# Kernel optimization log

Measured on AMD Instinct MI355X. Metric: run time of the kernel, lower is better.

Reference implementation:

```python
import jax, jax.numpy as jnp
import numpy as np

NUM_HEADS = 12
DIM_HEAD = 32
EMBED_DIM = NUM_HEADS * DIM_HEAD  # 384
EPS = 1e-5


def _channel_layernorm(x, w, b):
    # LayerNorm over channel axis (axis=1) of [B, D, S, L], per spatial position
    mu = jnp.mean(x, axis=1, keepdims=True)
    var = jnp.mean(jnp.square(x - mu), axis=1, keepdims=True)
    xn = (x - mu) / jnp.sqrt(var + EPS)
    return xn * w[None, :, None, None] + b[None, :, None, None]


def _qkv(x, w, b):
    # 1x1 conv == per-position matmul: [3D, D] x [B, D, S, L] -> [B, 3D, S, L]
    B, D, S, L = x.shape
    y = jnp.einsum('od,bdsl->bosl', w, x) + b[None, :, None, None]
    q, k, v = jnp.split(y, 3, axis=1)
    shp = (B, NUM_HEADS, DIM_HEAD, S, L)
    return q.reshape(shp), k.reshape(shp), v.reshape(shp)


def setup_inputs() -> dict:
    key = jax.random.key(0)
    ks = jax.random.split(key, 5)
    B, D, S, L = 1, EMBED_DIM, 128, 256
    x = jax.random.normal(ks[0], (B, D, S, L), dtype=jnp.float32)
    row_w = jax.random.normal(ks[1], (3 * D, D), dtype=jnp.float32) * (D ** -0.5)
    row_b = jax.random.normal(ks[2], (3 * D,), dtype=jnp.float32) * 0.02
    col_w = jax.random.normal(ks[3], (3 * D, D), dtype=jnp.float32) * (D ** -0.5)
    col_b = jax.random.normal(ks[4], (3 * D,), dtype=jnp.float32) * 0.02
    return {
        'x': x,
        'row_w': row_w, 'row_b': row_b,
        'col_w': col_w, 'col_b': col_b,
        'ln1_w': jnp.ones((D,), jnp.float32), 'ln1_b': jnp.zeros((D,), jnp.float32),
        'ln2_w': jnp.ones((D,), jnp.float32), 'ln2_b': jnp.zeros((D,), jnp.float32),
    }


def reference(x, row_w, row_b, col_w, col_b, ln1_w, ln1_b, ln2_w, ln2_b):
    B, D, S, L = x.shape
    # --- row attention (attend across L within each row s) ---
    q, k, v = _qkv(x, row_w, row_b)  # [B,H,C,S,L]
    row_attn = jnp.einsum('bhcsi,bhcsj->bhsij', q, k)  # note: no 1/sqrt(d) scaling (faithful)
    row_attn = jax.nn.softmax(row_attn, axis=-1)
    row_out = jnp.einsum('bhsij,bhdsj->bhdsi', row_attn, v).reshape(B, D, S, L)
    out = _channel_layernorm(x + row_out, ln1_w, ln1_b)
    # --- column attention (attend across S within each column l) ---
    q, k, v = _qkv(out, col_w, col_b)
    col_attn = jnp.einsum('bhcil,bhcjl->bhijl', q, k)
    col_attn = jax.nn.softmax(col_attn, axis=-2)
    col_out = jnp.einsum('bhijl,bhdjl->bhdil', col_attn, v).reshape(B, D, S, L)
    out = _channel_layernorm(out + col_out, ln2_w, ln2_b)
    return out
```

## Files before the change

kernel.cpp:

```cpp
#include <hip/hip_runtime.h>
#include <math.h>

#define DCH 384
#define NH 12
#define CH 32
#define SS 128
#define LL 256
#define NPOS 32768
#define THREE_D 1152

typedef _Float16 f16_t;
typedef _Float16 f16x4 __attribute__((ext_vector_type(4)));
typedef _Float16 f16x8 __attribute__((ext_vector_type(8)));
typedef float f32x4 __attribute__((ext_vector_type(4)));

#define GLD16(gptr, lptr) __builtin_amdgcn_global_load_lds( \
    (const __attribute__((address_space(1))) unsigned int*)(gptr), \
    (__attribute__((address_space(3))) unsigned int*)(lptr), 16, 0, 0)

#define WAVE_LDS_FENCE() __asm__ volatile("s_waitcnt lgkmcnt(0)" ::: "memory")

__global__ __launch_bounds__(256) void conv_w(const float* __restrict__ in,
                                              f16_t* __restrict__ out, int n4) {
    int i = blockIdx.x * 256 + threadIdx.x;
    if (i < n4) {
        float4 v = ((const float4*)in)[i];
        unsigned short u0 = __builtin_bit_cast(unsigned short, (f16_t)v.x);
        unsigned short u1 = __builtin_bit_cast(unsigned short, (f16_t)v.y);
        unsigned short u2 = __builtin_bit_cast(unsigned short, (f16_t)v.z);
        unsigned short u3 = __builtin_bit_cast(unsigned short, (f16_t)v.w);
        uint2 r;
        r.x = (unsigned)u0 | ((unsigned)u1 << 16);
        r.y = (unsigned)u2 | ((unsigned)u3 << 16);
        ((uint2*)out)[i] = r;
    }
}

__global__ __launch_bounds__(256) void zero_stats(float* __restrict__ p) {
    ((float4*)p)[blockIdx.x * 256 + threadIdx.x] = (float4){0.f, 0.f, 0.f, 0.f};
}

__global__ __launch_bounds__(256) void conv_xT(const float* __restrict__ in,
                                               f16_t* __restrict__ outp) {
    __shared__ float tile[64][65];
    const int p0 = blockIdx.x * 64;
    const int k0 = blockIdx.y * 64;
    const int tx = threadIdx.x & 63, ty = threadIdx.x >> 6;
#pragma unroll
    for (int i = 0; i < 16; ++i)
        tile[ty * 16 + i][tx] = in[(size_t)(k0 + ty * 16 + i) * NPOS + p0 + tx];
    __syncthreads();
    const int pr = threadIdx.x >> 2;
    const int cg = threadIdx.x & 3;
    union { uint4 v[2]; unsigned int u[8]; } res;
#pragma unroll
    for (int j = 0; j < 8; ++j) {
        unsigned short lo = __builtin_bit_cast(unsigned short, (f16_t)tile[cg * 16 + 2 * j][pr]);
        unsigned short hi = __builtin_bit_cast(unsigned short, (f16_t)tile[cg * 16 + 2 * j + 1][pr]);
        res.u[j] = (unsigned)lo | ((unsigned)hi << 16);
    }
    uint4* dst = (uint4*)&outp[(size_t)(p0 + pr) * DCH + k0 + cg * 16];
    dst[0] = res.v[0];
    dst[1] = res.v[1];
}

__global__ __launch_bounds__(512) void qkv_gemm_f16(
        const f16_t* __restrict__ Wh,
        const float* __restrict__ bias,
        const f16_t* __restrict__ Xp,
        f16_t* __restrict__ Yq, f16_t* __restrict__ Yk, f16_t* __restrict__ Yv)
{
    __shared__ f16_t sha[128 * 384];
    const int tid  = threadIdx.x;
    const int lane = tid & 63;
    const int wave = tid >> 6;

    const int hwid = blockIdx.y * 9 + blockIdx.x;
    const int nid  = (hwid & 7) * 144 + (hwid >> 3);
    const int ot   = nid % 9;
    const int pt   = nid / 9;
    const int o0 = ot * 128;
    const int p0 = pt * 256;

    const int mrow = lane & 15;
    const int kgq  = lane >> 4;

#pragma unroll
    for (int j = 0; j < 12; ++j) {
        const int ibase = (wave * 12 + j) * 64;
        const int i = ibase + lane;
        const int row = i / 48;
        const int s = i - row * 48;
        const int g = s ^ (row & 7);
        GLD16(Wh + (size_t)(o0 + row) * DCH + g * 8, sha + (size_t)ibase * 8);
    }

    const f16_t* bp0 = Xp + (size_t)(p0 + wave * 32 + mrow) * DCH + kgq * 8;
    const f16_t* bp1 = bp0 + (size_t)16 * DCH;

    f32x4 acc[8][2] = {};
    f16x8 breg[3][2];

    breg[0][0] = *(const f16x8*)(bp0);
    breg[0][1] = *(const f16x8*)(bp1);
    breg[1][0] = *(const f16x8*)(bp0 + 32);
    breg[1][1] = *(const f16x8*)(bp1 + 32);

    __syncthreads();

    const int key = mrow & 7;
    constexpr int NK = DCH / 32;
#pragma unroll
    for (int t = 0; t < NK; ++t) {
        if (t + 2 < NK) {
            breg[(t + 2) % 3][0] = *(const f16x8*)(bp0 + (t + 2) * 32);
            breg[(t + 2) % 3][1] = *(const f16x8*)(bp1 + (t + 2) * 32);
        }
        const int soff = ((t * 4 + kgq) ^ key) * 8;
#pragma unroll
        for (int mi = 0; mi < 8; ++mi) {
            const f16x8 a = *(const f16x8*)(sha + (size_t)(mi * 16 + mrow) * DCH + soff);
            acc[mi][0] = __builtin_amdgcn_mfma_f32_16x16x32_f16(
                a, breg[t % 3][0], acc[mi][0], 0, 0, 0);
            acc[mi][1] = __builtin_amdgcn_mfma_f32_16x16x32_f16(
                a, breg[t % 3][1], acc[mi][1], 0, 0, 0);
        }
    }

    const int col = lane & 15;
    const int rq4 = (lane >> 4) * 4;
    const int qkv = ot / 3;
    const int grp = ot % 3;

    if (qkv < 2) {
        f16_t* Yt = (qkv == 0) ? Yq : Yk;
#pragma unroll
        for (int mi = 0; mi < 8; ++mi) {
            const int h  = grp * 4 + (mi >> 1);
            const int cb = (mi & 1) * 16 + rq4;
            const int ob = o0 + mi * 16 + rq4;
            const float b0 = bias[ob], b1 = bias[ob + 1];
            const float b2 = bias[ob + 2], b3 = bias[ob + 3];
#pragma unroll
            for (int ni = 0; ni < 2; ++ni) {
                const int p = p0 + wave * 32 + ni * 16 + col;
                union { uint2 u; f16_t h4[4]; } w;
                w.h4[0] = (f16_t)(acc[mi][ni][0] + b0);
                w.h4[1] = (f16_t)(acc[mi][ni][1] + b1);
                w.h4[2] = (f16_t)(acc[mi][ni][2] + b2);
                w.h4[3] = (f16_t)(acc[mi][ni][3] + b3);
                *(uint2*)(Yt + ((size_t)h * NPOS + p) * CH + cb) = w.u;
            }
        }
    } else {
#pragma unroll
        for (int mi = 0; mi < 8; ++mi) {
#pragma unroll
            for (int r = 0; r < 4; ++r) {
                const int cg = grp * 128 + mi * 16 + rq4 + r;
                const float br = bias[768 + cg];
#pragma unroll
                for (int ni = 0; ni < 2; ++ni) {
                    const int p = p0 + wave * 32 + ni * 16 + col;
                    Yv[(size_t)cg * NPOS + p] = (f16_t)(acc[mi][ni][r] + br);
                }
            }
        }
    }
}

template <int SEQ, bool XT16>
__global__ __launch_bounds__(256) void mfma_attn(
        const f16_t* __restrict__ Yq, const f16_t* __restrict__ Yk,
        const f16_t* __restrict__ Yv, const void* __restrict__ Xv_,
        f16_t* __restrict__ R, float* __restrict__ SUM, float* __restrict__ SQ)
{
    constexpr int JT  = SEQ / 16;
    constexpr int NIT = SEQ / 64;
    constexpr int PST = SEQ + 8;
    constexpr int VST = SEQ + 8;
    __shared__ f16_t Ks[SEQ * CH];
    __shared__ f16_t Vs[CH * VST];
    __shared__ f16_t pb[4][16 * PST];
    const int tid  = threadIdx.x;
    const int lane = tid & 63;
    const int wave = tid >> 6;
    const int col = lane & 15, quad = lane >> 4;
    const int h = blockIdx.x % NH;
    const size_t pbase = (size_t)(blockIdx.x / NH) * SEQ;

    const f16_t* qg = Yq + ((size_t)h * NPOS + pbase) * CH;
    const f16_t* kg = Yk + ((size_t)h * NPOS + pbase) * CH;
    const f16_t* vg = Yv + (size_t)h * CH * NPOS + pbase;
    f16_t* mypb = pb[wave];

    {
        const int ksw = (lane & 3) ^ ((lane >> 3) & 3);
        const int lrow32 = (lane >> 2) * 32;
#pragma unroll
        for (int i = 0; i < SEQ / 64; ++i) {
            const int off = (wave * (SEQ / 64) + i) * 512;
            GLD16(kg + off + lrow32 + ksw * 8, Ks + off);
        }
    }
    {
        constexpr int CPR = SEQ / 8;
        const int vch = tid % CPR;
        const int vr0 = tid / CPR;
#pragma unroll
        for (int r = vr0; r < CH; r += 256 / CPR)
            *(float4*)(Vs + r * VST + vch * 8) =
                *(const float4*)(vg + (size_t)r * NPOS + vch * 8);
    }
    __syncthreads();

    const int kq8 = (quad ^ ((col >> 1) & 3)) * 8;

    for (int it = 0; it < NIT; ++it) {
        const int i0 = (wave * NIT + it) * 16;
        const f16x8 qf = *(const f16x8*)(qg + (size_t)(i0 + col) * CH + quad * 8);
        f32x4 st[JT];
#pragma unroll
        for (int mt = 0; mt < JT; ++mt) {
            f16x8 kf = *(const f16x8*)(Ks + (mt * 16 + col) * CH + kq8);
            st[mt] = __builtin_amdgcn_mfma_f32_16x16x32_f16(kf, qf, (f32x4){0.f, 0.f, 0.f, 0.f}, 0, 0, 0);
        }
        float sum = 0.f;
#pragma unroll
        for (int mt = 0; mt < JT; ++mt)
#pragma unroll
            for (int r = 0; r < 4; ++r) {
                st[mt][r] = __expf(st[mt][r]);
                sum += st[mt][r];
            }
        sum += __shfl_xor(sum, 16, 64);
        sum += __shfl_xor(sum, 32, 64);
        const float inv = 1.f / sum;
#pragma unroll
        for (int mt = 0; mt < JT; ++mt) {
            union { uint2 u; f16_t h4[4]; } w;
            w.h4[0] = (f16_t)(st[mt][0] * inv);
            w.h4[1] = (f16_t)(st[mt][1] * inv);
            w.h4[2] = (f16_t)(st[mt][2] * inv);
            w.h4[3] = (f16_t)(st[mt][3] * inv);
            *(uint2*)(mypb + col * PST + mt * 16 + quad * 4) = w.u;
        }
        WAVE_LDS_FENCE();

        f32x4 o0a = {0.f, 0.f, 0.f, 0.f}, o0b = {0.f, 0.f, 0.f, 0.f};
        f32x4 o1a = {0.f, 0.f, 0.f, 0.f}, o1b = {0.f, 0.f, 0.f, 0.f};
#pragma unroll
        for (int ks = 0; ks < SEQ / 32; ks += 2) {
            f16x8 pf0 = *(const f16x8*)(mypb + col * PST + ks * 32 + quad * 8);
            f16x8 pf1 = *(const f16x8*)(mypb + col * PST + (ks + 1) * 32 + quad * 8);
            f16x8 va0 = *(const f16x8*)(Vs + col * VST + ks * 32 + quad * 8);
            f16x8 va1 = *(const f16x8*)(Vs + col * VST + (ks + 1) * 32 + quad * 8);
            f16x8 vb0 = *(const f16x8*)(Vs + (16 + col) * VST + ks * 32 + quad * 8);
            f16x8 vb1 = *(const f16x8*)(Vs + (16 + col) * VST + (ks + 1) * 32 + quad * 8);
            o0a = __builtin_amdgcn_mfma_f32_16x16x32_f16(va0, pf0, o0a, 0, 0, 0);
            o0b = __builtin_amdgcn_mfma_f32_16x16x32_f16(va1, pf1, o0b, 0, 0, 0);
            o1a = __builtin_amdgcn_mfma_f32_16x16x32_f16(vb0, pf0, o1a, 0, 0, 0);
            o1b = __builtin_amdgcn_mfma_f32_16x16x32_f16(vb1, pf1, o1b, 0, 0, 0);
        }
        const f32x4 ot0 = o0a + o0b;
        const f32x4 ot1 = o1a + o1b;

        const size_t pos = pbase + i0 + col;
        float a0[4], a1[4];
        if constexpr (XT16) {
            const f16_t* Xh = (const f16_t*)Xv_;
            const f16x4 xa = *(const f16x4*)(Xh + pos * DCH + h * CH + quad * 4);
            const f16x4 xb = *(const f16x4*)(Xh + pos * DCH + h * CH + 16 + quad * 4);
#pragma unroll
            for (int r = 0; r < 4; ++r) {
                a0[r] = (float)xa[r] + ot0[r];
                a1[r] = (float)xb[r] + ot1[r];
            }
        } else {
            const float* Xf = (const float*)Xv_;
#pragma unroll
            for (int r = 0; r < 4; ++r) {
                a0[r] = Xf[(size_t)(h * CH + quad * 4 + r) * NPOS + pos] + ot0[r];
                a1[r] = Xf[(size_t)(h * CH + 16 + quad * 4 + r) * NPOS + pos] + ot1[r];
            }
        }
        float psum = 0.f, psq = 0.f;
#pragma unroll
        for (int r = 0; r < 4; ++r) {
            R[(size_t)(h * CH + quad * 4 + r) * NPOS + pos]      = (f16_t)a0[r];
            R[(size_t)(h * CH + 16 + quad * 4 + r) * NPOS + pos] = (f16_t)a1[r];
            psum += a0[r] + a1[r];
            psq  += a0[r] * a0[r] + a1[r] * a1[r];
        }
        psum += __shfl_xor(psum, 16, 64);
        psum += __shfl_xor(psum, 32, 64);
        psq  += __shfl_xor(psq, 16, 64);
        psq  += __shfl_xor(psq, 32, 64);
        if (quad == 0) {
            atomicAdd(&SUM[pos], psum);
            atomicAdd(&SQ[pos], psq);
        }
    }
}

__global__ __launch_bounds__(256) void norm_xT(
        const f16_t* __restrict__ A, const float* __restrict__ SUM,
        const float* __restrict__ SQ, const float* __restrict__ w,
        const float* __restrict__ b, f16_t* __restrict__ Xp) {
    __shared__ float tile[64][65];
    const int l0 = (blockIdx.x & 3) * 64;
    const int s  = (blockIdx.x >> 2) & (SS - 1);
    const int k0 = (blockIdx.x >> 9) * 64;
    const int tx = threadIdx.x & 63, ty = threadIdx.x >> 6;
    const int pos0 = s * LL + l0;
    const float m  = SUM[pos0 + tx] * (1.f / DCH);
    const float rs = rsqrtf(SQ[pos0 + tx] * (1.f / DCH) - m * m + 1e-5f);
#pragma unroll
    for (int i = 0; i < 16; ++i) {
        const int d = k0 + ty * 16 + i;
        float v = (float)A[(size_t)d * NPOS + pos0 + tx];
        tile[ty * 16 + i][tx] = (v - m) * rs * w[d] + b[d];
    }
    __syncthreads();
    const int pr = threadIdx.x >> 2;
    const int cg = threadIdx.x & 3;
    union { uint4 v[2]; unsigned int u[8]; } res;
#pragma unroll
    for (int j = 0; j < 8; ++j) {
        unsigned short lo = __builtin_bit_cast(unsigned short, (f16_t)tile[cg * 16 + 2 * j][pr]);
        unsigned short hi = __builtin_bit_cast(unsigned short, (f16_t)tile[cg * 16 + 2 * j + 1][pr]);
        res.u[j] = (unsigned)lo | ((unsigned)hi << 16);
    }
    uint4* dst = (uint4*)&Xp[(size_t)((l0 + pr) * SS + s) * DCH + k0 + cg * 16];
    dst[0] = res.v[0];
    dst[1] = res.v[1];
}

__global__ __launch_bounds__(256) void norm_transpose(
        const f16_t* __restrict__ in, const float* __restrict__ SUM,
        const float* __restrict__ SQ, const float* __restrict__ w,
        const float* __restrict__ b, float* __restrict__ out, int Rr, int Cc) {
    __shared__ float tile[32][33];
    const int ntc = Cc >> 5, ntr = Rr >> 5;
    int tc = blockIdx.x % ntc;
    int tr = (blockIdx.x / ntc) % ntr;
    int d = blockIdx.x / (ntc * ntr);
    int tx = threadIdx.x & 31, ty = threadIdx.x >> 5;
    const f16_t* ip = in + (size_t)d * Rr * Cc;
    float* op = out + (size_t)d * Rr * Cc;
    const float wd = w[d], bd = b[d];
#pragma unroll
    for (int i = 0; i < 32; i += 8) {
        const int r = tr * 32 + ty + i;
        const int c = tc * 32 + tx;
        const int pos = r * Cc + c;
        const float m  = SUM[pos] * (1.f / DCH);
        const float rs = rsqrtf(SQ[pos] * (1.f / DCH) - m * m + 1e-5f);
        float v = (float)ip[(size_t)r * Cc + c];
        tile[ty + i][tx] = (v - m) * rs * wd + bd;
    }
    __syncthreads();
#pragma unroll
    for (int i = 0; i < 32; i += 8)
        op[(size_t)(tc * 32 + ty + i) * Rr + tr * 32 + tx] = tile[tx][ty + i];
}

extern "C" void kernel_launch(void* const* d_in, const int* in_sizes, int n_in,
                              void* d_out, int out_size, void* d_ws, size_t ws_size,
                              hipStream_t stream) {
    const float* x     = (const float*)d_in[0];
    const float* row_w = (const float*)d_in[1];
    const float* row_b = (const float*)d_in[2];
    const float* col_w = (const float*)d_in[3];
    const float* col_b = (const float*)d_in[4];
    const float* ln1_w = (const float*)d_in[5];
    const float* ln1_b = (const float*)d_in[6];
    const float* ln2_w = (const float*)d_in[7];
    const float* ln2_b = (const float*)d_in[8];
    float* out = (float*)d_out;

    char* ws = (char*)d_ws;
    const size_t ysz = (size_t)NH * NPOS * CH * 2;
    const size_t abytes = (size_t)DCH * NPOS * 4;
    f16_t* Yq = (f16_t*)ws;
    f16_t* Yk = (f16_t*)(ws + ysz);
    f16_t* Yv = (f16_t*)(ws + 2 * ysz);
    f16_t* A  = (f16_t*)(ws + 3 * ysz);
    f16_t* Xp = (f16_t*)(ws + 3 * ysz + abytes);
    f16_t* Wh = (f16_t*)(ws + 3 * ysz + abytes + ysz);
    float* SUMB = (float*)(ws + 3 * ysz + abytes + ysz + (1 << 21));
    float* SQB  = SUMB + NPOS;

    dim3 ggrid(THREE_D / 128, NPOS / 256);
    const int wn4 = THREE_D * DCH / 4;
    dim3 cgrid(NPOS / 64, DCH / 64);

    conv_w<<<(wn4 + 255) / 256, 256, 0, stream>>>(row_w, Wh, wn4);
    conv_xT<<<cgrid, 256, 0, stream>>>(x, Xp);
    zero_stats<<<2 * NPOS / 1024, 256, 0, stream>>>(SUMB);
    qkv_gemm_f16<<<ggrid, 512, 0, stream>>>(Wh, row_b, Xp, Yq, Yk, Yv);
    mfma_attn<LL, false><<<NH * SS, 256, 0, stream>>>(Yq, Yk, Yv, x, A, SUMB, SQB);
    norm_xT<<<(DCH / 64) * SS * (LL / 64), 256, 0, stream>>>(A, SUMB, SQB, ln1_w, ln1_b, Xp);

    conv_w<<<(wn4 + 255) / 256, 256, 0, stream>>>(col_w, Wh, wn4);
    zero_stats<<<2 * NPOS / 1024, 256, 0, stream>>>(SUMB);
    qkv_gemm_f16<<<ggrid, 512, 0, stream>>>(Wh, col_b, Xp, Yq, Yk, Yv);
    mfma_attn<SS, true><<<NH * LL, 256, 0, stream>>>(Yq, Yk, Yv, Xp, A, SUMB, SQB);
    norm_transpose<<<DCH * (LL / 32) * (SS / 32), 256, 0, stream>>>(
        A, SUMB, SQB, ln2_w, ln2_b, out, LL, SS);
}
```

Before: 320.7 us.

## Use position-major layouts in row attention and simplify LN1 to row-wise

Row attention now reads its residual from the fp16 position-major Xp buffer instead of the fp32 channel-major input, and writes its pre-norm output position-major with vector stores. This lets the first layernorm become a plain row-wise kernel with 16-byte loads and stores instead of an LDS tile transpose. The QKV GEMM's LDS swizzle is widened from 8 to 16 rows to cut bank conflicts. The residual now comes from an fp16 copy of x, which reduces precision slightly.

```diff
diff --git a/kernel.cpp b/kernel.cpp
--- a/kernel.cpp
+++ b/kernel.cpp
@@ -91,7 +91,7 @@
         const int i = ibase + lane;
         const int row = i / 48;
         const int s = i - row * 48;
-        const int g = s ^ (row & 7);
+        const int g = s ^ (row & 15);
         GLD16(Wh + (size_t)(o0 + row) * DCH + g * 8, sha + (size_t)ibase * 8);
     }
 
@@ -108,7 +108,6 @@
 
     __syncthreads();
 
-    const int key = mrow & 7;
     constexpr int NK = DCH / 32;
 #pragma unroll
     for (int t = 0; t < NK; ++t) {
@@ -116,10 +115,11 @@
             breg[(t + 2) % 3][0] = *(const f16x8*)(bp0 + (t + 2) * 32);
             breg[(t + 2) % 3][1] = *(const f16x8*)(bp1 + (t + 2) * 32);
         }
-        const int soff = ((t * 4 + kgq) ^ key) * 8;
+        const int soff = ((t * 4 + kgq) ^ mrow) * 8;
 #pragma unroll
         for (int mi = 0; mi < 8; ++mi) {
-            const f16x8 a = *(const f16x8*)(sha + (size_t)(mi * 16 + mrow) * DCH + soff);
+            const f16x8 a = *(const f16x8*)(
+                sha + (size_t)(mi * 16 + mrow) * DCH + soff);
             acc[mi][0] = __builtin_amdgcn_mfma_f32_16x16x32_f16(
                 a, breg[t % 3][0], acc[mi][0], 0, 0, 0);
             acc[mi][1] = __builtin_amdgcn_mfma_f32_16x16x32_f16(
@@ -169,10 +169,10 @@
     }
 }
 
-template <int SEQ, bool XT16>
+template <int SEQ, bool AROW>
 __global__ __launch_bounds__(256) void mfma_attn(
         const f16_t* __restrict__ Yq, const f16_t* __restrict__ Yk,
-        const f16_t* __restrict__ Yv, const void* __restrict__ Xv_,
+        const f16_t* __restrict__ Yv, const f16_t* __restrict__ Xh,
         f16_t* __restrict__ R, float* __restrict__ SUM, float* __restrict__ SQ)
 {
     constexpr int JT  = SEQ / 16;
@@ -266,31 +266,35 @@
         const f32x4 ot1 = o1a + o1b;
 
         const size_t pos = pbase + i0 + col;
+        const f16x4 xa = *(const f16x4*)(Xh + pos * DCH + h * CH + quad * 4);
+        const f16x4 xb = *(const f16x4*)(Xh + pos * DCH + h * CH + 16 + quad * 4);
         float a0[4], a1[4];
-        if constexpr (XT16) {
-            const f16_t* Xh = (const f16_t*)Xv_;
-            const f16x4 xa = *(const f16x4*)(Xh + pos * DCH + h * CH + quad * 4);
-            const f16x4 xb = *(const f16x4*)(Xh + pos * DCH + h * CH + 16 + quad * 4);
-#pragma unroll
-            for (int r = 0; r < 4; ++r) {
-                a0[r] = (float)xa[r] + ot0[r];
-                a1[r] = (float)xb[r] + ot1[r];
-            }
-        } else {
-            const float* Xf = (const float*)Xv_;
-#pragma unroll
-            for (int r = 0; r < 4; ++r) {
-                a0[r] = Xf[(size_t)(h * CH + quad * 4 + r) * NPOS + pos] + ot0[r];
-                a1[r] = Xf[(size_t)(h * CH + 16 + quad * 4 + r) * NPOS + pos] + ot1[r];
-            }
+#pragma unroll
+        for (int r = 0; r < 4; ++r) {
+            a0[r] = (float)xa[r] + ot0[r];
+            a1[r] = (float)xb[r] + ot1[r];
         }
         float psum = 0.f, psq = 0.f;
 #pragma unroll
         for (int r = 0; r < 4; ++r) {
-            R[(size_t)(h * CH + quad * 4 + r) * NPOS + pos]      = (f16_t)a0[r];
-            R[(size_t)(h * CH + 16 + quad * 4 + r) * NPOS + pos] = (f16_t)a1[r];
             psum += a0[r] + a1[r];
             psq  += a0[r] * a0[r] + a1[r] * a1[r];
+        }
+        if constexpr (AROW) {
+            f16x4 w0, w1;
+#pragma unroll
+            for (int r = 0; r < 4; ++r) {
+                w0[r] = (f16_t)a0[r];
+                w1[r] = (f16_t)a1[r];
+            }
+            *(f16x4*)(R + pos * DCH + h * CH + quad * 4)      = w0;
+            *(f16x4*)(R + pos * DCH + h * CH + 16 + quad * 4) = w1;
+        } else {
+#pragma unroll
+            for (int r = 0; r < 4; ++r) {
+                R[(size_t)(h * CH + quad * 4 + r) * NPOS + pos]      = (f16_t)a0[r];
+                R[(size_t)(h * CH + 16 + quad * 4 + r) * NPOS + pos] = (f16_t)a1[r];
+            }
         }
         psum += __shfl_xor(psum, 16, 64);
         psum += __shfl_xor(psum, 32, 64);
@@ -307,33 +311,33 @@
         const f16_t* __restrict__ A, const float* __restrict__ SUM,
         const float* __restrict__ SQ, const float* __restrict__ w,
         const float* __restrict__ b, f16_t* __restrict__ Xp) {
-    __shared__ float tile[64][65];
-    const int l0 = (blockIdx.x & 3) * 64;
-    const int s  = (blockIdx.x >> 2) & (SS - 1);
-    const int k0 = (blockIdx.x >> 9) * 64;
-    const int tx = threadIdx.x & 63, ty = threadIdx.x >> 6;
-    const int pos0 = s * LL + l0;
-    const float m  = SUM[pos0 + tx] * (1.f / DCH);
-    const float rs = rsqrtf(SQ[pos0 + tx] * (1.f / DCH) - m * m + 1e-5f);
-#pragma unroll
-    for (int i = 0; i < 16; ++i) {
-        const int d = k0 + ty * 16 + i;
-        float v = (float)A[(size_t)d * NPOS + pos0 + tx];
-        tile[ty * 16 + i][tx] = (v - m) * rs * w[d] + b[d];
-    }
-    __syncthreads();
-    const int pr = threadIdx.x >> 2;
-    const int cg = threadIdx.x & 3;
-    union { uint4 v[2]; unsigned int u[8]; } res;
-#pragma unroll
-    for (int j = 0; j < 8; ++j) {
-        unsigned short lo = __builtin_bit_cast(unsigned short, (f16_t)tile[cg * 16 + 2 * j][pr]);
-        unsigned short hi = __builtin_bit_cast(unsigned short, (f16_t)tile[cg * 16 + 2 * j + 1][pr]);
-        res.u[j] = (unsigned)lo | ((unsigned)hi << 16);
-    }
-    uint4* dst = (uint4*)&Xp[(size_t)((l0 + pr) * SS + s) * DCH + k0 + cg * 16];
-    dst[0] = res.v[0];
-    dst[1] = res.v[1];
+    const int row = blockIdx.x * 64 + (threadIdx.x >> 2);
+    const int c4 = threadIdx.x & 3;
+    const int s = row >> 8, l = row & (LL - 1);
+    const int po = l * SS + s;
+    const float m  = SUM[row] * (1.f / DCH);
+    const float rs = rsqrtf(SQ[row] * (1.f / DCH) - m * m + 1e-5f);
+    const f16_t* ar = A + (size_t)row * DCH;
+    f16_t* xr = Xp + (size_t)po * DCH;
+#pragma unroll
+    for (int j = 0; j < 12; ++j) {
+        const int d0 = c4 * 8 + j * 32;
+        f16x8 v = *(const f16x8*)(ar + d0);
+        const float4 w0 = *(const float4*)(w + d0);
+        const float4 w1 = *(const float4*)(w + d0 + 4);
+        const float4 b0 = *(const float4*)(b + d0);
+        const float4 b1 = *(const float4*)(b + d0 + 4);
+        f16x8 o;
+        o[0] = (f16_t)(((float)v[0] - m) * rs * w0.x + b0.x);
+        o[1] = (f16_t)(((float)v[1] - m) * rs * w0.y + b0.y);
+        o[2] = (f16_t)(((float)v[2] - m) * rs * w0.z + b0.z);
+        o[3] = (f16_t)(((float)v[3] - m) * rs * w0.w + b0.w);
+        o[4] = (f16_t)(((float)v[4] - m) * rs * w1.x + b1.x);
+        o[5] = (f16_t)(((float)v[5] - m) * rs * w1.y + b1.y);
+        o[6] = (f16_t)(((float)v[6] - m) * rs * w1.z + b1.z);
+        o[7] = (f16_t)(((float)v[7] - m) * rs * w1.w + b1.w);
+        *(f16x8*)(xr + d0) = o;
+    }
 }
 
 __global__ __launch_bounds__(256) void norm_transpose(
@@ -399,13 +403,13 @@
     conv_xT<<<cgrid, 256, 0, stream>>>(x, Xp);
     zero_stats<<<2 * NPOS / 1024, 256, 0, stream>>>(SUMB);
     qkv_gemm_f16<<<ggrid, 512, 0, stream>>>(Wh, row_b, Xp, Yq, Yk, Yv);
-    mfma_attn<LL, false><<<NH * SS, 256, 0, stream>>>(Yq, Yk, Yv, x, A, SUMB, SQB);
-    norm_xT<<<(DCH / 64) * SS * (LL / 64), 256, 0, stream>>>(A, SUMB, SQB, ln1_w, ln1_b, Xp);
+    mfma_attn<LL, true><<<NH * SS, 256, 0, stream>>>(Yq, Yk, Yv, Xp, A, SUMB, SQB);
+    norm_xT<<<NPOS / 64, 256, 0, stream>>>(A, SUMB, SQB, ln1_w, ln1_b, Xp);
 
     conv_w<<<(wn4 + 255) / 256, 256, 0, stream>>>(col_w, Wh, wn4);
     zero_stats<<<2 * NPOS / 1024, 256, 0, stream>>>(SUMB);
     qkv_gemm_f16<<<ggrid, 512, 0, stream>>>(Wh, col_b, Xp, Yq, Yk, Yv);
-    mfma_attn<SS, true><<<NH * LL, 256, 0, stream>>>(Yq, Yk, Yv, Xp, A, SUMB, SQB);
+    mfma_attn<SS, false><<<NH * LL, 256, 0, stream>>>(Yq, Yk, Yv, Xp, A, SUMB, SQB);
     norm_transpose<<<DCH * (LL / 32) * (SS / 32), 256, 0, stream>>>(
         A, SUMB, SQB, ln2_w, ln2_b, out, LL, SS);
 }
```

Measured after the change: 323.5 us. No clear change (+0.9%).
